# Kernel tuning notes

Measured on AMD Instinct MI355X. Metric: run time of the kernel, lower is better.

The kernel has to match this reference:

```python
import jax, jax.numpy as jnp
import numpy as np


def _conv2d(x, w, pad):
    return jax.lax.conv_general_dilated(
        x, w, (1, 1), [(pad, pad), (pad, pad)],
        dimension_numbers=('NCHW', 'OIHW', 'NCHW'))


def _affine_grid(theta, k):
    # torch F.affine_grid, align_corners=False; output size (k, k)
    base = ((2.0 * jnp.arange(k) + 1.0) / k - 1.0).astype(jnp.float32)
    pts = jnp.stack([
        jnp.broadcast_to(base[None, :], (k, k)),  # x varies along width
        jnp.broadcast_to(base[:, None], (k, k)),  # y varies along height
        jnp.ones((k, k), jnp.float32)], -1)        # [k,k,3]
    return jnp.einsum('ijc,nrc->nijr', pts, theta)  # [N,k,k,2] -> (x,y)


def _grid_sample(img, grid):
    # torch F.grid_sample: bilinear, zeros padding, align_corners=False
    # img [C,H,W], grid [k,k,2] with (x,y) in [-1,1]
    C, H, W = img.shape
    gx = (grid[..., 0] + 1.0) * W * 0.5 - 0.5
    gy = (grid[..., 1] + 1.0) * H * 0.5 - 0.5
    x0 = jnp.floor(gx); y0 = jnp.floor(gy)
    wx = gx - x0; wy = gy - y0
    x0i = x0.astype(jnp.int32); y0i = y0.astype(jnp.int32)

    def gath(yi, xi):
        valid = ((xi >= 0) & (xi < W) & (yi >= 0) & (yi < H)).astype(img.dtype)
        v = img[:, jnp.clip(yi, 0, H - 1), jnp.clip(xi, 0, W - 1)]  # [C,k,k]
        return v * valid[None]

    v00 = gath(y0i, x0i); v01 = gath(y0i, x0i + 1)
    v10 = gath(y0i + 1, x0i); v11 = gath(y0i + 1, x0i + 1)
    return (v00 * ((1 - wx) * (1 - wy))[None] + v01 * (wx * (1 - wy))[None]
            + v10 * ((1 - wx) * wy)[None] + v11 * (wx * wy)[None])


def reference(x, stn0_w, stn0_b, stn1_w, lin_w, lin_b, check):
    B, C, H, W = x.shape
    k = stn1_w.shape[-1]
    h = jax.nn.relu(_conv2d(x, stn0_w, k // 2) + stn0_b[None, :, None, None])
    ident6 = jnp.array([1., 0., 0., 0., 1., 0.], jnp.float32)
    out = _conv2d(h, stn1_w, 0) * (1.0 - check) + ident6[None, :, None, None]
    Ho, Wo = out.shape[2], out.shape[3]
    N = B * Ho * Wo
    # permute(0,3,2,1).view(N,2,3) as in torch
    theta = out.transpose(0, 3, 2, 1).reshape(N, 2, 3)
    grid = _affine_grid(theta, k)  # [N,k,k,2]
    xv = jnp.arange(k // 2, k // 2 + Ho, dtype=jnp.float32)[:, None]  # meshgrid 'ij'
    yv = jnp.arange(k // 2, k // 2 + Wo, dtype=jnp.float32)[None, :]
    half = float(k // 2)
    auxx = ((grid[..., 0] * half).reshape(B, Ho, Wo, k, k)
            + xv[None, :, :, None, None]).reshape(N, k, k) / (H - 1) * 2.0 - 1.0
    auxy = ((grid[..., 1] * half).reshape(B, Ho, Wo, k, k)
            + yv[None, :, :, None, None]).reshape(N, k, k) / (W - 1) * 2.0 - 1.0
    auxgrid = jnp.stack([auxx, auxy], -1).reshape(B, Ho * Wo, k, k, 2)
    # tile(x,0,Ho*Wo) duplicates x[b] for each of its Ho*Wo grids; gather directly
    xs = jax.vmap(lambda img, g: jax.vmap(lambda gg: _grid_sample(img, gg))(g))(x, auxgrid)  # [B,P,C,k,k]
    x_out = xs.reshape(N, -1) @ lin_w.T + lin_b  # [N,O]
    score = x_out.reshape(B, Ho, Wo, -1).transpose(0, 3, 2, 1)  # [B,O,Wo,Ho] as in torch
    ident23 = jnp.array([[1., 0., 0.], [0., 1., 0.]], jnp.float32)
    return score, ident23[None] - theta, out, auxx, auxy


def setup_inputs() -> dict:
    key = jax.random.key(0)
    ks = jax.random.split(key, 6)
    C, O, k = 128, 256, 3
    B, H, W = 8, 56, 56
    x = jax.random.normal(ks[0], (B, C, H, W), jnp.float32)
    stn0_w = jax.random.normal(ks[1], (C, C, k, k), jnp.float32) * (1.0 / np.sqrt(C * k * k))
    stn0_b = jax.random.normal(ks[2], (C,), jnp.float32) * 0.01
    # original zero-inits stn1; use small random so theta is non-trivial
    stn1_w = jax.random.normal(ks[3], (6, C, k, k), jnp.float32) * 0.01
    lin_w = jax.random.normal(ks[4], (O, C * k * k), jnp.float32) * (1.0 / np.sqrt(C * k * k))
    lin_b = jax.random.normal(ks[5], (O,), jnp.float32) * 0.01
    return {'x': x, 'stn0_w': stn0_w, 'stn0_b': stn0_b, 'stn1_w': stn1_w,
            'lin_w': lin_w, 'lin_b': lin_b, 'check': 0}
```

## Files before the change

kernel.cpp:

```cpp
#include <hip/hip_runtime.h>

typedef __attribute__((ext_vector_type(4))) float f32x4;
typedef __attribute__((ext_vector_type(8))) short bf16x8;

#define OPLANE 2916
#define NN 23328
#define KDIM 1152
#define PLANE 3136
#define LDP 72

__device__ __forceinline__ unsigned short f2bf(float f) {
    unsigned u = __builtin_bit_cast(unsigned, f);
    u += 0x7fffu + ((u >> 16) & 1u);
    return (unsigned short)(u >> 16);
}

__global__ __launch_bounds__(256) void k_prep(const float* __restrict__ w0,
                                              const float* __restrict__ lw,
                                              unsigned short* __restrict__ b1t,
                                              unsigned short* __restrict__ b2t) {
    int idx = blockIdx.x * 256 + threadIdx.x;
    if (idx < 147456) {
        int r = idx / KDIM, k = idx - r * KDIM;
        int ij = k >> 7, ic = k & 127;
        b1t[idx] = f2bf(w0[r * KDIM + ic * 9 + ij]);
    } else {
        int j = idx - 147456;
        int r = j / KDIM, k = j - r * KDIM;
        int ij = k >> 7, ic = k & 127;
        b2t[j] = f2bf(lw[r * KDIM + ic * 9 + ij]);
    }
}

__global__ __launch_bounds__(256) void k_nhwc(const float* __restrict__ x,
                                              unsigned short* __restrict__ xnh) {
    __shared__ unsigned short lds[56 * 132];
    const int y = blockIdx.x, b = blockIdx.y, tid = threadIdx.x;
    for (int i = tid; i < 7168; i += 256) {
        int ic = i / 56, xc = i - ic * 56;
        lds[xc * 132 + ic] = f2bf(x[(b * 128 + ic) * PLANE + y * 56 + xc]);
    }
    __syncthreads();
    for (int i = tid; i < 7168; i += 256) {
        int xc = i >> 7, ic = i & 127;
        xnh[(b * PLANE + y * 56 + xc) * 128 + ic] = lds[xc * 132 + ic];
    }
}

__global__ __launch_bounds__(256) void k_gemm1(const unsigned short* __restrict__ xnh,
                                               const unsigned short* __restrict__ Bt,
                                               const float* __restrict__ bias,
                                               float* __restrict__ C) {
    __shared__ unsigned short As[64 * LDP];
    __shared__ unsigned short Bs[64 * LDP];
    const int tid = threadIdx.x;
    const int lane = tid & 63, wid = tid >> 6;
    const int wr = wid >> 1, wc = wid & 1;
    const int n0 = blockIdx.x * 64;
    const int m0 = blockIdx.y * 64;

    f32x4 acc[2][2];
    #pragma unroll
    for (int mt = 0; mt < 2; mt++)
        #pragma unroll
        for (int nt = 0; nt < 2; nt++) { acc[mt][nt][0]=0.f; acc[mt][nt][1]=0.f; acc[mt][nt][2]=0.f; acc[mt][nt][3]=0.f; }

    const int row = tid >> 2, q = tid & 3;
    const int p = m0 + row;
    const int b = p / PLANE; int rem = p - b * PLANE;
    const int y = rem / 56; const int xc = rem - y * 56;
    unsigned short* asw = &As[row * LDP + q * 16];
    const unsigned short* bg = Bt + (n0 + row) * KDIM + q * 16;
    unsigned short* bsw = &Bs[row * LDP + q * 16];
    const int lm = lane & 15, lq = lane >> 4;

    uint4 a0, a1, bv0, bv1;
    auto issue = [&](int it) {
        const int ij = it >> 1;
        const int di = ij / 3, dj = ij - di * 3;
        const int icb = (it & 1) << 6;
        a0 = make_uint4(0u,0u,0u,0u); a1 = make_uint4(0u,0u,0u,0u);
        bool valid = (y + di >= 1) && (y + di <= 56) && (xc + dj >= 1) && (xc + dj <= 56);
        if (valid) {
            const unsigned short* ap = xnh + (p + (di - 1) * 56 + (dj - 1)) * 128 + icb + q * 16;
            a0 = *(const uint4*)ap;
            a1 = *(const uint4*)(ap + 8);
        }
        bv0 = *(const uint4*)(bg + it * 64);
        bv1 = *(const uint4*)(bg + it * 64 + 8);
    };
    issue(0);

    #pragma unroll
    for (int it = 0; it < 18; it++) {
        __syncthreads();
        *(uint4*)(asw + 0) = a0;  *(uint4*)(asw + 8) = a1;
        *(uint4*)(bsw + 0) = bv0; *(uint4*)(bsw + 8) = bv1;
        __syncthreads();
        if (it < 17) issue(it + 1);
        #pragma unroll
        for (int kk = 0; kk < 64; kk += 32) {
            bf16x8 af[2], bf[2];
            #pragma unroll
            for (int mt = 0; mt < 2; mt++)
                af[mt] = *(const bf16x8*)&As[(wr * 32 + mt * 16 + lm) * LDP + kk + lq * 8];
            #pragma unroll
            for (int nt = 0; nt < 2; nt++)
                bf[nt] = *(const bf16x8*)&Bs[(wc * 32 + nt * 16 + lm) * LDP + kk + lq * 8];
            #pragma unroll
            for (int mt = 0; mt < 2; mt++)
                #pragma unroll
                for (int nt = 0; nt < 2; nt++)
                    acc[mt][nt] = __builtin_amdgcn_mfma_f32_16x16x32_bf16(af[mt], bf[nt], acc[mt][nt], 0, 0, 0);
        }
    }
    #pragma unroll
    for (int mt = 0; mt < 2; mt++) {
        int m = m0 + wr * 32 + mt * 16 + lq * 4;
        #pragma unroll
        for (int nt = 0; nt < 2; nt++) {
            int n = n0 + wc * 32 + nt * 16 + lm;
            float bb = bias[n];
            #pragma unroll
            for (int r = 0; r < 4; r++)
                C[(m + r) * 128 + n] = fmaxf(acc[mt][nt][r] + bb, 0.f);
        }
    }
}

__global__ __launch_bounds__(256) void k_conv2f(const float* __restrict__ h,
                                                const float* __restrict__ w1,
                                                const int* __restrict__ check,
                                                float* __restrict__ o_out,
                                                float* __restrict__ o_th,
                                                float* __restrict__ o_ax,
                                                float* __restrict__ o_ay,
                                                float* __restrict__ sxy) {
    __shared__ float wlds[6912];
    __shared__ float red[16 * 6 * 17];
    __shared__ float vals[96];
    const int tid = threadIdx.x;
    for (int idx = tid; idx < 6912; idx += 256) {
        int r = idx / KDIM, k = idx - r * KDIM;
        int ij = k >> 7, ic = k & 127;
        wlds[idx] = w1[r * KDIM + ic * 9 + ij];
    }
    __syncthreads();
    const int pt = tid >> 4, c = tid & 15;
    const int p = blockIdx.x * 16 + pt;
    int b = p / OPLANE; int rem = p - b * OPLANE; int oh = rem / 54; int ow = rem - oh * 54;
    const float4* h4 = (const float4*)h;
    const float4* w4 = (const float4*)wlds;
    float acc[6] = {0.f, 0.f, 0.f, 0.f, 0.f, 0.f};
    const int base_sp = b * PLANE + oh * 56 + ow;
    #pragma unroll
    for (int i = 0; i < 3; i++) {
        #pragma unroll
        for (int j = 0; j < 3; j++) {
            int sp = base_sp + i * 56 + j;
            float4 h0 = h4[sp * 32 + c * 2];
            float4 h1 = h4[sp * 32 + c * 2 + 1];
            int ij = i * 3 + j;
            #pragma unroll
            for (int r = 0; r < 6; r++) {
                float4 wa = w4[r * 288 + ij * 32 + c * 2];
                float4 wb = w4[r * 288 + ij * 32 + c * 2 + 1];
                acc[r] += h0.x * wa.x + h0.y * wa.y + h0.z * wa.z + h0.w * wa.w
                        + h1.x * wb.x + h1.y * wb.y + h1.z * wb.z + h1.w * wb.w;
            }
        }
    }
    #pragma unroll
    for (int r = 0; r < 6; r++) red[(pt * 6 + r) * 17 + c] = acc[r];
    __syncthreads();
    if (tid < 96) {
        const float* rp = &red[tid * 17];
        float s = 0.f;
        #pragma unroll
        for (int e = 0; e < 16; e++) s += rp[e];
        vals[tid] = s;
    }
    __syncthreads();
    if (tid < 16) {
        int p2 = blockIdx.x * 16 + tid;
        int b2 = p2 / OPLANE; int r2 = p2 - b2 * OPLANE; int oh2 = r2 / 54; int ow2 = r2 - oh2 * 54;
        float val[6];
        float s = 1.0f - (float)check[0];
        const float id6[6] = {1.f, 0.f, 0.f, 0.f, 1.f, 0.f};
        #pragma unroll
        for (int r = 0; r < 6; r++) val[r] = vals[tid * 6 + r] * s + id6[r];
        int n = (b2 * 54 + ow2) * 54 + oh2;
        #pragma unroll
        for (int r = 0; r < 6; r++) {
            o_out[((b2 * 6 + r) * 54 + oh2) * 54 + ow2] = val[r];
            o_th[n * 6 + r] = id6[r] - val[r];
        }
        const float bse[3] = {-2.f / 3.f, 0.f, 2.f / 3.f};
        #pragma unroll
        for (int i = 0; i < 3; i++)
            #pragma unroll
            for (int j = 0; j < 3; j++) {
                float gx = bse[j] * val[0] + bse[i] * val[1] + val[2];
                float gy = bse[j] * val[3] + bse[i] * val[4] + val[5];
                float ax = (gx + 1.f + (float)ow2) * (2.f / 55.f) - 1.f;
                float ay = (gy + 1.f + (float)oh2) * (2.f / 55.f) - 1.f;
                int ij = i * 3 + j;
                o_ax[n * 9 + ij] = ax;
                o_ay[n * 9 + ij] = ay;
                sxy[(n * 9 + ij) * 2 + 0] = (ax + 1.f) * 28.f - 0.5f;
                sxy[(n * 9 + ij) * 2 + 1] = (ay + 1.f) * 28.f - 0.5f;
            }
    }
}

__global__ __launch_bounds__(256) void k_sgemm(const unsigned short* __restrict__ xnh,
                                               const unsigned short* __restrict__ Wt,
                                               const float* __restrict__ bias,
                                               const float* __restrict__ sxy,
                                               float* __restrict__ score) {
    __shared__ unsigned short Ss[2][32 * LDP];
    const int tid = threadIdx.x;
    const int lane = tid & 63, wid = tid >> 6;
    const int s0 = blockIdx.x * 32;

    f32x4 acc[4][2];
    #pragma unroll
    for (int mt = 0; mt < 4; mt++)
        #pragma unroll
        for (int nt = 0; nt < 2; nt++) { acc[mt][nt][0]=0.f; acc[mt][nt][1]=0.f; acc[mt][nt][2]=0.f; acc[mt][nt][3]=0.f; }

    const int row = tid >> 3, q = tid & 7;
    const int mp = s0 + row;
    const int b = mp / OPLANE; const int rr = mp - b * OPLANE;
    const int ho = rr / 54, wo = rr - (rr / 54) * 54;
    const int n = (b * 54 + wo) * 54 + ho;
    const int xbase = b * PLANE;
    unsigned short* ssw0 = &Ss[0][row * LDP + q * 8];
    unsigned short* ssw1 = &Ss[1][row * LDP + q * 8];
    const int lm = lane & 15, lq = lane >> 4;
    const unsigned short* wgb = Wt + (wid * 64 + lm) * KDIM + lq * 8;

    float2 sc[9];
    {
        const float* spp = sxy + n * 18;
        #pragma unroll
        for (int ij = 0; ij < 9; ij++) sc[ij] = *(const float2*)(spp + ij * 2);
    }

    int off0 = 0, off1 = 0, off2 = 0, off3 = 0;
    float wt0 = 0.f, wt1 = 0.f, wt2 = 0.f, wt3 = 0.f;
    auto mkoff = [&](int ij) {
        float sx = sc[ij].x, sy = sc[ij].y;
        float x0f = floorf(sx), y0f = floorf(sy);
        float wx = sx - x0f, wy = sy - y0f;
        int x0 = (int)x0f, y0 = (int)y0f;
        int x1 = x0 + 1, y1 = y0 + 1;
        float vx0 = (x0 >= 0 && x0 < 56) ? 1.f : 0.f;
        float vx1 = (x1 >= 0 && x1 < 56) ? 1.f : 0.f;
        float vy0 = (y0 >= 0 && y0 < 56) ? 1.f : 0.f;
        float vy1 = (y1 >= 0 && y1 < 56) ? 1.f : 0.f;
        int xc0 = min(max(x0, 0), 55), xc1 = min(max(x1, 0), 55);
        int yc0 = min(max(y0, 0), 55), yc1 = min(max(y1, 0), 55);
        off0 = (xbase + yc0 * 56 + xc0) << 7;
        off1 = (xbase + yc0 * 56 + xc1) << 7;
        off2 = (xbase + yc1 * 56 + xc0) << 7;
        off3 = (xbase + yc1 * 56 + xc1) << 7;
        wt0 = vy0 * vx0 * (1.f - wx) * (1.f - wy);
        wt1 = vy0 * vx1 * wx * (1.f - wy);
        wt2 = vy1 * vx0 * (1.f - wx) * wy;
        wt3 = vy1 * vx1 * wx * wy;
    };

    uint4 p0, p1, p2, p3;
    auto issue = [&](int it) {
        const int co = ((it & 1) << 6) + q * 8;
        p0 = *(const uint4*)(xnh + off0 + co);
        p1 = *(const uint4*)(xnh + off1 + co);
        p2 = *(const uint4*)(xnh + off2 + co);
        p3 = *(const uint4*)(xnh + off3 + co);
    };
    auto blendv = [&]() -> uint4 {
        unsigned dwv[4];
        const unsigned* c0 = (const unsigned*)&p0;
        const unsigned* c1 = (const unsigned*)&p1;
        const unsigned* c2 = (const unsigned*)&p2;
        const unsigned* c3 = (const unsigned*)&p3;
        #pragma unroll
        for (int d = 0; d < 4; d++) {
            unsigned u0 = c0[d], u1 = c1[d], u2 = c2[d], u3 = c3[d];
            float lo = wt0 * __builtin_bit_cast(float, u0 << 16)
                     + wt1 * __builtin_bit_cast(float, u1 << 16)
                     + wt2 * __builtin_bit_cast(float, u2 << 16)
                     + wt3 * __builtin_bit_cast(float, u3 << 16);
            float hi = wt0 * __builtin_bit_cast(float, u0 & 0xffff0000u)
                     + wt1 * __builtin_bit_cast(float, u1 & 0xffff0000u)
                     + wt2 * __builtin_bit_cast(float, u2 & 0xffff0000u)
                     + wt3 * __builtin_bit_cast(float, u3 & 0xffff0000u);
            dwv[d] = (unsigned)f2bf(lo) | ((unsigned)f2bf(hi) << 16);
        }
        return *(uint4*)dwv;
    };

    mkoff(0);
    issue(0);
    *(uint4*)ssw0 = blendv();
    __syncthreads();

    #pragma unroll
    for (int it = 0; it < 18; it++) {
        const int cur = it & 1;
        if (it < 17) {
            if ((((it + 1) & 1)) == 0) mkoff((it + 1) >> 1);
            issue(it + 1);
        }
        #pragma unroll
        for (int kk = 0; kk < 64; kk += 32) {
            bf16x8 wf[4], sf[2];
            #pragma unroll
            for (int mt = 0; mt < 4; mt++)
                wf[mt] = *(const bf16x8*)(wgb + mt * 16 * KDIM + it * 64 + kk);
            #pragma unroll
            for (int nt = 0; nt < 2; nt++)
                sf[nt] = *(const bf16x8*)&Ss[cur][(nt * 16 + lm) * LDP + kk + lq * 8];
            #pragma unroll
            for (int mt = 0; mt < 4; mt++)
                #pragma unroll
                for (int nt = 0; nt < 2; nt++)
                    acc[mt][nt] = __builtin_amdgcn_mfma_f32_16x16x32_bf16(wf[mt], sf[nt], acc[mt][nt], 0, 0, 0);
        }
        if (it < 17) {
            *(uint4*)(cur ? ssw0 : ssw1) = blendv();
            __syncthreads();
        }
    }
    #pragma unroll
    for (int mt = 0; mt < 4; mt++) {
        #pragma unroll
        for (int r = 0; r < 4; r++) {
            int o = wid * 64 + mt * 16 + lq * 4 + r;
            float bb = bias[o];
            #pragma unroll
            for (int nt = 0; nt < 2; nt++) {
                int s = s0 + nt * 16 + lm;
                int sb = s / OPLANE;
                int soff = s - sb * OPLANE;
                score[(sb * 256 + o) * OPLANE + soff] = acc[mt][nt][r] + bb;
            }
        }
    }
}

extern "C" void kernel_launch(void* const* d_in, const int* in_sizes, int n_in,
                              void* d_out, int out_size, void* d_ws, size_t ws_size,
                              hipStream_t stream) {
    const float* x  = (const float*)d_in[0];
    const float* w0 = (const float*)d_in[1];
    const float* b0 = (const float*)d_in[2];
    const float* w1 = (const float*)d_in[3];
    const float* lw = (const float*)d_in[4];
    const float* lb = (const float*)d_in[5];
    const int* check = (const int*)d_in[6];

    float* out   = (float*)d_out;
    float* score = out;
    float* o_th  = out + 5971968;
    float* o_out = out + 6111936;
    float* o_ax  = out + 6251904;
    float* o_ay  = out + 6461856;

    char* wsb = (char*)d_ws;
    float* h   = (float*)wsb;
    unsigned short* xnh = (unsigned short*)(wsb + 12845056);
    unsigned short* b1t = (unsigned short*)(wsb + 19267584);
    unsigned short* b2t = (unsigned short*)(wsb + 19562496);
    float* sxy = (float*)(wsb + 20152320);

    k_prep<<<1728, 256, 0, stream>>>(w0, lw, b1t, b2t);
    k_nhwc<<<dim3(56, 8), 256, 0, stream>>>(x, xnh);
    k_gemm1<<<dim3(2, 392), 256, 0, stream>>>(xnh, b1t, b0, h);
    k_conv2f<<<1458, 256, 0, stream>>>(h, w1, check, o_out, o_th, o_ax, o_ay, sxy);
    k_sgemm<<<729, 256, 0, stream>>>(xnh, b2t, lb, sxy, score);
}
```

Before: 185.7 us.

## Retile sampling GEMM to 128x64 blocks with LDS-staged weights

Restructures the grid-sample+linear GEMM so each block computes 128 outputs by 64 samples. Weights are staged through shared memory with a 128-wide K step per bilinear tap, instead of every wave reading weight fragments straight from global memory. The grid splits output channels across two blocks, so each block blends half as many output columns per sample. The price is that the bilinear gather and blend run twice, once per output half. Double buffering is replaced by a single buffer guarded by two barriers, with register prefetch of the next tap, and a bounds guard is added for the ragged last tile.

```diff
diff --git a/kernel.cpp b/kernel.cpp
--- a/kernel.cpp
+++ b/kernel.cpp
@@ -8,6 +8,7 @@
 #define KDIM 1152
 #define PLANE 3136
 #define LDP 72
+#define LDP2 136
 
 __device__ __forceinline__ unsigned short f2bf(float f) {
     unsigned u = __builtin_bit_cast(unsigned, f);
@@ -218,10 +219,13 @@
                                                const float* __restrict__ bias,
                                                const float* __restrict__ sxy,
                                                float* __restrict__ score) {
-    __shared__ unsigned short Ss[2][32 * LDP];
+    __shared__ unsigned short Ss[64 * LDP2];
+    __shared__ unsigned short Ws[128 * LDP2];
     const int tid = threadIdx.x;
     const int lane = tid & 63, wid = tid >> 6;
-    const int s0 = blockIdx.x * 32;
+    const int wr = wid >> 1, wc = wid & 1;
+    const int o0 = blockIdx.x * 128;
+    const int s0 = blockIdx.y * 64;
 
     f32x4 acc[4][2];
     #pragma unroll
@@ -229,16 +233,17 @@
         #pragma unroll
         for (int nt = 0; nt < 2; nt++) { acc[mt][nt][0]=0.f; acc[mt][nt][1]=0.f; acc[mt][nt][2]=0.f; acc[mt][nt][3]=0.f; }
 
-    const int row = tid >> 3, q = tid & 7;
-    const int mp = s0 + row;
+    const int row = tid >> 2, q = tid & 3;
+    const int mp = min(s0 + row, NN - 1);
     const int b = mp / OPLANE; const int rr = mp - b * OPLANE;
     const int ho = rr / 54, wo = rr - (rr / 54) * 54;
     const int n = (b * 54 + wo) * 54 + ho;
     const int xbase = b * PLANE;
-    unsigned short* ssw0 = &Ss[0][row * LDP + q * 8];
-    unsigned short* ssw1 = &Ss[1][row * LDP + q * 8];
+    unsigned short* ssw = &Ss[row * LDP2 + q * 32];
+    const int wrow = tid >> 1, wq = tid & 1;
+    const unsigned short* wg = Wt + (o0 + wrow) * KDIM + wq * 64;
+    unsigned short* wsw = &Ws[wrow * LDP2 + wq * 64];
     const int lm = lane & 15, lq = lane >> 4;
-    const unsigned short* wgb = Wt + (wid * 64 + lm) * KDIM + lq * 8;
 
     float2 sc[9];
     {
@@ -271,23 +276,39 @@
         wt3 = vy1 * vx1 * wx * wy;
     };
 
-    uint4 p0, p1, p2, p3;
-    auto issue = [&](int it) {
-        const int co = ((it & 1) << 6) + q * 8;
-        p0 = *(const uint4*)(xnh + off0 + co);
-        p1 = *(const uint4*)(xnh + off1 + co);
-        p2 = *(const uint4*)(xnh + off2 + co);
-        p3 = *(const uint4*)(xnh + off3 + co);
+    uint4 g0a, g0b, g1a, g1b, g2a, g2b, g3a, g3b;
+    uint4 t0a, t0b, t1a, t1b, t2a, t2b, t3a, t3b;
+    uint4 w0v, w1v, w2v, w3v, w4v, w5v, w6v, w7v;
+    auto issue = [&](int ij) {
+        const int co = q * 32;
+        g0a = *(const uint4*)(xnh + off0 + co);      g0b = *(const uint4*)(xnh + off0 + co + 8);
+        g1a = *(const uint4*)(xnh + off1 + co);      g1b = *(const uint4*)(xnh + off1 + co + 8);
+        g2a = *(const uint4*)(xnh + off2 + co);      g2b = *(const uint4*)(xnh + off2 + co + 8);
+        g3a = *(const uint4*)(xnh + off3 + co);      g3b = *(const uint4*)(xnh + off3 + co + 8);
+        t0a = *(const uint4*)(xnh + off0 + co + 16); t0b = *(const uint4*)(xnh + off0 + co + 24);
+        t1a = *(const uint4*)(xnh + off1 + co + 16); t1b = *(const uint4*)(xnh + off1 + co + 24);
+        t2a = *(const uint4*)(xnh + off2 + co + 16); t2b = *(const uint4*)(xnh + off2 + co + 24);
+        t3a = *(const uint4*)(xnh + off3 + co + 16); t3b = *(const uint4*)(xnh + off3 + co + 24);
+        const unsigned short* wp = wg + ij * 128;
+        w0v = *(const uint4*)(wp + 0);
+        w1v = *(const uint4*)(wp + 8);
+        w2v = *(const uint4*)(wp + 16);
+        w3v = *(const uint4*)(wp + 24);
+        w4v = *(const uint4*)(wp + 32);
+        w5v = *(const uint4*)(wp + 40);
+        w6v = *(const uint4*)(wp + 48);
+        w7v = *(const uint4*)(wp + 56);
     };
-    auto blendv = [&]() -> uint4 {
+
+    auto blend4 = [&](const uint4& c0, const uint4& c1, const uint4& c2, const uint4& c3) -> uint4 {
         unsigned dwv[4];
-        const unsigned* c0 = (const unsigned*)&p0;
-        const unsigned* c1 = (const unsigned*)&p1;
-        const unsigned* c2 = (const unsigned*)&p2;
-        const unsigned* c3 = (const unsigned*)&p3;
+        const unsigned* u0p = (const unsigned*)&c0;
+        const unsigned* u1p = (const unsigned*)&c1;
+        const unsigned* u2p = (const unsigned*)&c2;
+        const unsigned* u3p = (const unsigned*)&c3;
         #pragma unroll
         for (int d = 0; d < 4; d++) {
-            unsigned u0 = c0[d], u1 = c1[d], u2 = c2[d], u3 = c3[d];
+            unsigned u0 = u0p[d], u1 = u1p[d], u2 = u2p[d], u3 = u3p[d];
             float lo = wt0 * __builtin_bit_cast(float, u0 << 16)
                      + wt1 * __builtin_bit_cast(float, u1 << 16)
                      + wt2 * __builtin_bit_cast(float, u2 << 16)
@@ -298,53 +319,66 @@
                      + wt3 * __builtin_bit_cast(float, u3 & 0xffff0000u);
             dwv[d] = (unsigned)f2bf(lo) | ((unsigned)f2bf(hi) << 16);
         }
-        return *(uint4*)dwv;
+        return *(const uint4*)dwv;
     };
 
     mkoff(0);
     issue(0);
-    *(uint4*)ssw0 = blendv();
-    __syncthreads();
-
-    #pragma unroll
-    for (int it = 0; it < 18; it++) {
-        const int cur = it & 1;
-        if (it < 17) {
-            if ((((it + 1) & 1)) == 0) mkoff((it + 1) >> 1);
+
+    #pragma unroll
+    for (int it = 0; it < 9; it++) {
+        uint4 o0v = blend4(g0a, g1a, g2a, g3a);
+        uint4 o1v = blend4(g0b, g1b, g2b, g3b);
+        uint4 o2v = blend4(t0a, t1a, t2a, t3a);
+        uint4 o3v = blend4(t0b, t1b, t2b, t3b);
+        __syncthreads();
+        *(uint4*)(ssw + 0)  = o0v;
+        *(uint4*)(ssw + 8)  = o1v;
+        *(uint4*)(ssw + 16) = o2v;
+        *(uint4*)(ssw + 24) = o3v;
+        *(uint4*)(wsw + 0)  = w0v;
+        *(uint4*)(wsw + 8)  = w1v;
+        *(uint4*)(wsw + 16) = w2v;
+        *(uint4*)(wsw + 24) = w3v;
+        *(uint4*)(wsw + 32) = w4v;
+        *(uint4*)(wsw + 40) = w5v;
+        *(uint4*)(wsw + 48) = w6v;
+        *(uint4*)(wsw + 56) = w7v;
+        __syncthreads();
+        if (it < 8) {
+            mkoff(it + 1);
             issue(it + 1);
         }
         #pragma unroll
-        for (int kk = 0; kk < 64; kk += 32) {
+        for (int kk = 0; kk < 128; kk += 32) {
             bf16x8 wf[4], sf[2];
             #pragma unroll
             for (int mt = 0; mt < 4; mt++)
-                wf[mt] = *(const bf16x8*)(wgb + mt * 16 * KDIM + it * 64 + kk);
+                wf[mt] = *(const bf16x8*)&Ws[(wr * 64 + mt * 16 + lm) * LDP2 + kk + lq * 8];
             #pragma unroll
             for (int nt = 0; nt < 2; nt++)
-                sf[nt] = *(const bf16x8*)&Ss[cur][(nt * 16 + lm) * LDP + kk + lq * 8];
+                sf[nt] = *(const bf16x8*)&Ss[(wc * 32 + nt * 16 + lm) * LDP2 + kk + lq * 8];
             #pragma unroll
             for (int mt = 0; mt < 4; mt++)
                 #pragma unroll
                 for (int nt = 0; nt < 2; nt++)
                     acc[mt][nt] = __builtin_amdgcn_mfma_f32_16x16x32_bf16(wf[mt], sf[nt], acc[mt][nt], 0, 0, 0);
         }
-        if (it < 17) {
-            *(uint4*)(cur ? ssw0 : ssw1) = blendv();
-            __syncthreads();
-        }
     }
     #pragma unroll
     for (int mt = 0; mt < 4; mt++) {
         #pragma unroll
         for (int r = 0; r < 4; r++) {
-            int o = wid * 64 + mt * 16 + lq * 4 + r;
+            int o = o0 + wr * 64 + mt * 16 + lq * 4 + r;
             float bb = bias[o];
             #pragma unroll
             for (int nt = 0; nt < 2; nt++) {
-                int s = s0 + nt * 16 + lm;
-                int sb = s / OPLANE;
-                int soff = s - sb * OPLANE;
-                score[(sb * 256 + o) * OPLANE + soff] = acc[mt][nt][r] + bb;
+                int s = s0 + wc * 32 + nt * 16 + lm;
+                if (s < NN) {
+                    int sb = s / OPLANE;
+                    int soff = s - sb * OPLANE;
+                    score[(sb * 256 + o) * OPLANE + soff] = acc[mt][nt][r] + bb;
+                }
             }
         }
     }
@@ -379,5 +413,5 @@
     k_nhwc<<<dim3(56, 8), 256, 0, stream>>>(x, xnh);
     k_gemm1<<<dim3(2, 392), 256, 0, stream>>>(xnh, b1t, b0, h);
     k_conv2f<<<1458, 256, 0, stream>>>(h, w1, check, o_out, o_th, o_ax, o_ay, sxy);
-    k_sgemm<<<729, 256, 0, stream>>>(xnh, b2t, lb, sxy, score);
-}
+    k_sgemm<<<dim3(2, 365), 256, 0, stream>>>(xnh, b2t, lb, sxy, score);
+}
```

Measured after the change: 200.3 us. 1.08x slower.

## Stage weight tiles in LDS and use 512-thread blocks in sampling GEMM

Applied to the files above, without the earlier changes.

The sampling GEMM kernel now loads each 256x64 weight tile cooperatively into shared memory and has 8 waves read it from there, instead of each wave pulling its weight fragments straight from global memory. The block grows to 512 threads, with waves split 4x2 over output channels and sample columns. Each thread now gathers and blends 4 channels instead of 8. The LDS double buffer is replaced by a single buffer guarded by two barriers per iteration, so global loads overlap less with MFMA work and synchronisation cost goes up.

```diff
diff --git a/kernel.cpp b/kernel.cpp
--- a/kernel.cpp
+++ b/kernel.cpp
@@ -213,32 +213,34 @@
     }
 }
 
-__global__ __launch_bounds__(256) void k_sgemm(const unsigned short* __restrict__ xnh,
+__global__ __launch_bounds__(512) void k_sgemm(const unsigned short* __restrict__ xnh,
                                                const unsigned short* __restrict__ Wt,
                                                const float* __restrict__ bias,
                                                const float* __restrict__ sxy,
                                                float* __restrict__ score) {
-    __shared__ unsigned short Ss[2][32 * LDP];
+    __shared__ unsigned short Ss[32 * LDP];
+    __shared__ unsigned short Ws[256 * LDP];
     const int tid = threadIdx.x;
     const int lane = tid & 63, wid = tid >> 6;
+    const int wr = wid >> 1;
+    const int wc = wid & 1;
     const int s0 = blockIdx.x * 32;
 
-    f32x4 acc[4][2];
-    #pragma unroll
-    for (int mt = 0; mt < 4; mt++)
-        #pragma unroll
-        for (int nt = 0; nt < 2; nt++) { acc[mt][nt][0]=0.f; acc[mt][nt][1]=0.f; acc[mt][nt][2]=0.f; acc[mt][nt][3]=0.f; }
-
-    const int row = tid >> 3, q = tid & 7;
+    f32x4 acc[4];
+    #pragma unroll
+    for (int mt = 0; mt < 4; mt++) { acc[mt][0]=0.f; acc[mt][1]=0.f; acc[mt][2]=0.f; acc[mt][3]=0.f; }
+
+    const int row = tid >> 4, q = tid & 15;
     const int mp = s0 + row;
     const int b = mp / OPLANE; const int rr = mp - b * OPLANE;
     const int ho = rr / 54, wo = rr - (rr / 54) * 54;
     const int n = (b * 54 + wo) * 54 + ho;
     const int xbase = b * PLANE;
-    unsigned short* ssw0 = &Ss[0][row * LDP + q * 8];
-    unsigned short* ssw1 = &Ss[1][row * LDP + q * 8];
+    unsigned short* ssw = &Ss[row * LDP + q * 4];
+    const int wrow = tid >> 1, wq = tid & 1;
+    const unsigned short* wg = Wt + wrow * KDIM + wq * 32;
+    unsigned short* wsw = &Ws[wrow * LDP + wq * 32];
     const int lm = lane & 15, lq = lane >> 4;
-    const unsigned short* wgb = Wt + (wid * 64 + lm) * KDIM + lq * 8;
 
     float2 sc[9];
     {
@@ -271,23 +273,30 @@
         wt3 = vy1 * vx1 * wx * wy;
     };
 
-    uint4 p0, p1, p2, p3;
+    uint2 p0, p1, p2, p3;
+    uint4 w0v, w1v, w2v, w3v;
     auto issue = [&](int it) {
-        const int co = ((it & 1) << 6) + q * 8;
-        p0 = *(const uint4*)(xnh + off0 + co);
-        p1 = *(const uint4*)(xnh + off1 + co);
-        p2 = *(const uint4*)(xnh + off2 + co);
-        p3 = *(const uint4*)(xnh + off3 + co);
+        const int co = ((it & 1) << 6) + q * 4;
+        p0 = *(const uint2*)(xnh + off0 + co);
+        p1 = *(const uint2*)(xnh + off1 + co);
+        p2 = *(const uint2*)(xnh + off2 + co);
+        p3 = *(const uint2*)(xnh + off3 + co);
+        const unsigned short* wp = wg + it * 64;
+        w0v = *(const uint4*)(wp + 0);
+        w1v = *(const uint4*)(wp + 8);
+        w2v = *(const uint4*)(wp + 16);
+        w3v = *(const uint4*)(wp + 24);
     };
-    auto blendv = [&]() -> uint4 {
-        unsigned dwv[4];
-        const unsigned* c0 = (const unsigned*)&p0;
-        const unsigned* c1 = (const unsigned*)&p1;
-        const unsigned* c2 = (const unsigned*)&p2;
-        const unsigned* c3 = (const unsigned*)&p3;
-        #pragma unroll
-        for (int d = 0; d < 4; d++) {
-            unsigned u0 = c0[d], u1 = c1[d], u2 = c2[d], u3 = c3[d];
+
+    auto blend2 = [&]() -> uint2 {
+        unsigned dwv[2];
+        const unsigned* u0p = (const unsigned*)&p0;
+        const unsigned* u1p = (const unsigned*)&p1;
+        const unsigned* u2p = (const unsigned*)&p2;
+        const unsigned* u3p = (const unsigned*)&p3;
+        #pragma unroll
+        for (int d = 0; d < 2; d++) {
+            unsigned u0 = u0p[d], u1 = u1p[d], u2 = u2p[d], u3 = u3p[d];
             float lo = wt0 * __builtin_bit_cast(float, u0 << 16)
                      + wt1 * __builtin_bit_cast(float, u1 << 16)
                      + wt2 * __builtin_bit_cast(float, u2 << 16)
@@ -298,54 +307,49 @@
                      + wt3 * __builtin_bit_cast(float, u3 & 0xffff0000u);
             dwv[d] = (unsigned)f2bf(lo) | ((unsigned)f2bf(hi) << 16);
         }
-        return *(uint4*)dwv;
+        uint2 r; r.x = dwv[0]; r.y = dwv[1];
+        return r;
     };
 
     mkoff(0);
     issue(0);
-    *(uint4*)ssw0 = blendv();
-    __syncthreads();
 
     #pragma unroll
     for (int it = 0; it < 18; it++) {
-        const int cur = it & 1;
+        uint2 sv = blend2();
+        __syncthreads();
+        *(uint2*)ssw = sv;
+        *(uint4*)(wsw + 0)  = w0v;
+        *(uint4*)(wsw + 8)  = w1v;
+        *(uint4*)(wsw + 16) = w2v;
+        *(uint4*)(wsw + 24) = w3v;
+        __syncthreads();
         if (it < 17) {
-            if ((((it + 1) & 1)) == 0) mkoff((it + 1) >> 1);
+            if (((it + 1) & 1) == 0) mkoff((it + 1) >> 1);
             issue(it + 1);
         }
         #pragma unroll
         for (int kk = 0; kk < 64; kk += 32) {
-            bf16x8 wf[4], sf[2];
+            bf16x8 wf[4], sf;
             #pragma unroll
             for (int mt = 0; mt < 4; mt++)
-                wf[mt] = *(const bf16x8*)(wgb + mt * 16 * KDIM + it * 64 + kk);
-            #pragma unroll
-            for (int nt = 0; nt < 2; nt++)
-                sf[nt] = *(const bf16x8*)&Ss[cur][(nt * 16 + lm) * LDP + kk + lq * 8];
+                wf[mt] = *(const bf16x8*)&Ws[(wr * 64 + mt * 16 + lm) * LDP + kk + lq * 8];
+            sf = *(const bf16x8*)&Ss[(wc * 16 + lm) * LDP + kk + lq * 8];
             #pragma unroll
             for (int mt = 0; mt < 4; mt++)
-                #pragma unroll
-                for (int nt = 0; nt < 2; nt++)
-                    acc[mt][nt] = __builtin_amdgcn_mfma_f32_16x16x32_bf16(wf[mt], sf[nt], acc[mt][nt], 0, 0, 0);
-        }
-        if (it < 17) {
-            *(uint4*)(cur ? ssw0 : ssw1) = blendv();
-            __syncthreads();
+                acc[mt] = __builtin_amdgcn_mfma_f32_16x16x32_bf16(wf[mt], sf, acc[mt], 0, 0, 0);
         }
     }
     #pragma unroll
     for (int mt = 0; mt < 4; mt++) {
         #pragma unroll
         for (int r = 0; r < 4; r++) {
-            int o = wid * 64 + mt * 16 + lq * 4 + r;
+            int o = wr * 64 + mt * 16 + lq * 4 + r;
             float bb = bias[o];
-            #pragma unroll
-            for (int nt = 0; nt < 2; nt++) {
-                int s = s0 + nt * 16 + lm;
-                int sb = s / OPLANE;
-                int soff = s - sb * OPLANE;
-                score[(sb * 256 + o) * OPLANE + soff] = acc[mt][nt][r] + bb;
-            }
+            int s = s0 + wc * 16 + lm;
+            int sb = s / OPLANE;
+            int soff = s - sb * OPLANE;
+            score[(sb * 256 + o) * OPLANE + soff] = acc[mt][r] + bb;
         }
     }
 }
@@ -379,5 +383,5 @@
     k_nhwc<<<dim3(56, 8), 256, 0, stream>>>(x, xnh);
     k_gemm1<<<dim3(2, 392), 256, 0, stream>>>(xnh, b1t, b0, h);
     k_conv2f<<<1458, 256, 0, stream>>>(h, w1, check, o_out, o_th, o_ax, o_ay, sxy);
-    k_sgemm<<<729, 256, 0, stream>>>(xnh, b2t, lb, sxy, score);
-}
+    k_sgemm<<<729, 512, 0, stream>>>(xnh, b2t, lb, sxy, score);
+}
```

Result: faster. 175.8 us (-5.3%).
